# Kernel tuning notes

Measured on AMD Instinct MI355X. Metric: run time of the kernel, lower is better.

## Reference

```python
import jax, jax.numpy as jnp
import numpy as np
from jax import lax

WS = 11          # window_size
SIGMA = 1.5
CH = 3
PAD = WS // 2


def _depthwise_conv(x, w, groups):
    # x: [B, C, H, W], w: [C_out, C_in/groups, kh, kw]
    return lax.conv_general_dilated(
        x, w, window_strides=(1, 1), padding=[(PAD, PAD), (PAD, PAD)],
        feature_group_count=groups,
        dimension_numbers=("NCHW", "OIHW", "NCHW"))


def _make_window():
    xs = jnp.arange(WS, dtype=jnp.float32) - (WS // 2)
    g = jnp.exp(-(xs ** 2) / (2.0 * SIGMA ** 2))
    g = g / g.sum()
    w2d = jnp.outer(g, g)                       # [WS, WS]
    return jnp.broadcast_to(w2d, (CH, 1, WS, WS))  # depthwise kernel


def setup_inputs() -> dict:
    key = jax.random.key(0)
    k1, k2, k3 = jax.random.split(key, 3)
    B, H, W = 16, 512, 512
    img1 = jax.random.uniform(k1, (B, CH, H, W), dtype=jnp.float32)
    img2 = jax.random.uniform(k2, (B, CH, H, W), dtype=jnp.float32)
    match = jax.random.uniform(k3, (B, 1, H, W), dtype=jnp.float32)
    return {"img1": img1, "img2": img2, "match": match}


def reference(img1, img2, match):
    window = _make_window()
    box = jnp.ones((1, 1, WS, WS), dtype=jnp.float32) / (WS * WS)

    # mask from match map: box-filter then threshold
    m = _depthwise_conv(match, box, 1) + 1e-07
    mask = (m > 0.5).astype(jnp.float32) + 1e-07   # [B,1,H,W]

    mu1 = _depthwise_conv(img1, window, CH)
    mu2 = _depthwise_conv(img2, window, CH)
    mu1_sq = mu1 * mu1
    mu2_sq = mu2 * mu2
    mu1_mu2 = mu1 * mu2
    sigma1_sq = _depthwise_conv(img1 * img1, window, CH) - mu1_sq
    sigma2_sq = _depthwise_conv(img2 * img2, window, CH) - mu2_sq
    sigma12 = _depthwise_conv(img1 * img2, window, CH) - mu1_mu2

    C1 = 0.01 ** 2
    C2 = 0.03 ** 2
    ssim_map = ((2 * mu1_mu2 + C1) * (2 * sigma12 + C2)) / (
        (mu1_sq + mu2_sq + C1) * (sigma1_sq + sigma2_sq + C2))

    # mask [B,1,H,W] broadcasts over the 3 channels of ssim_map
    return jnp.sum((1.0 - ssim_map) * mask) / jnp.sum(mask) / 3.0
```

## Files before the change

kernel.cpp:

```cpp
#include <hip/hip_runtime.h>


#define BATCH 16
#define CHANS 3
#define IMH 512
#define IMW 512
#define STRIPW 64
#define STRIPH 256
#define RINGR 18
#define LDSW 84
#define SUP 8
#define NSUP (STRIPH / SUP)
#define NQ 20

__device__ __forceinline__ float4 ld4s(const float* p) { return *(const float4*)p; }
__device__ __forceinline__ void st4s(float* p, float4 v) { *(float4*)p = v; }
__device__ __forceinline__ void fma4(float4& a, float w, float4 x) {
    a.x = fmaf(w, x.x, a.x); a.y = fmaf(w, x.y, a.y);
    a.z = fmaf(w, x.z, a.z); a.w = fmaf(w, x.w, a.w);
}
__device__ __forceinline__ void fma4m(float4& a, float w, float4 x, float4 y) {
    a.x = fmaf(w, x.x * y.x, a.x); a.y = fmaf(w, x.y * y.y, a.y);
    a.z = fmaf(w, x.z * y.z, a.z); a.w = fmaf(w, x.w * y.w, a.w);
}
__device__ __forceinline__ void add4(float4& a, float4 x) {
    a.x += x.x; a.y += x.y; a.z += x.z; a.w += x.w;
}

__device__ __forceinline__ void convg(const float* __restrict__ row, int cb,
                                      const float* __restrict__ g, float out[4]) {
    float w[20];
    #pragma unroll
    for (int i = 0; i < 5; ++i) {
        float4 v = ld4s(row + cb + 4 * i);
        w[4*i+0] = v.x; w[4*i+1] = v.y; w[4*i+2] = v.z; w[4*i+3] = v.w;
    }
    #pragma unroll
    for (int j = 0; j < 4; ++j) {
        float a = 0.0f;
        #pragma unroll
        for (int k = 0; k < 11; ++k) a = fmaf(g[k], w[3 + j + k], a);
        out[j] = a;
    }
}

__device__ __forceinline__ void convb(const float* __restrict__ row, int cb,
                                      float out[4]) {
    float w[20];
    #pragma unroll
    for (int i = 0; i < 5; ++i) {
        float4 v = ld4s(row + cb + 4 * i);
        w[4*i+0] = v.x; w[4*i+1] = v.y; w[4*i+2] = v.z; w[4*i+3] = v.w;
    }
    #pragma unroll
    for (int j = 0; j < 4; ++j) {
        float a = 0.0f;
        #pragma unroll
        for (int k = 0; k < 11; ++k) a += w[3 + j + k];
        out[j] = a;
    }
}

__global__ __launch_bounds__(256) void ssim_main(
    const float* __restrict__ img1, const float* __restrict__ img2,
    const float* __restrict__ match, double* __restrict__ acc)
{
    __shared__ __align__(16) float ring1[RINGR][LDSW];
    __shared__ __align__(16) float ring2[RINGR][LDSW];
    __shared__ __align__(16) float ringm[RINGR][LDSW];
    __shared__ __align__(16) float fld[6][SUP][LDSW];
    __shared__ float redn[4], redd[4];

    const int tid = threadIdx.x;
    const int bc = blockIdx.z;
    const int b = bc / CHANS;
    const int c = bc - b * CHANS;
    const int ystart = blockIdx.y * STRIPH;
    const int bx0 = blockIdx.x * STRIPW - 8;

    const float* p1 = img1 + (size_t)(b * CHANS + c) * (IMH * IMW);
    const float* p2 = img2 + (size_t)(b * CHANS + c) * (IMH * IMW);
    const float* pm = match + (size_t)b * (IMH * IMW);

    float g[11];
    {
        float s = 0.0f;
        #pragma unroll
        for (int i = 0; i < 11; ++i) {
            float d = (float)(i - 5);
            g[i] = expf(-(d * d) / 4.5f);
            s += g[i];
        }
        #pragma unroll
        for (int i = 0; i < 11; ++i) g[i] /= s;
    }

    float num = 0.0f, den = 0.0f;

    auto stage = [&](int gy0, int nrows) {
        for (int t = tid; t < nrows * NQ; t += 256) {
            int r = t / NQ, q = t - r * NQ;
            int gy = gy0 + r;
            int slot = (gy + 36) % RINGR;
            int gx = bx0 + 4 * q;
            float4 v1, v2, vm;
            if ((unsigned)gy < IMH && (unsigned)gx <= (IMW - 4)) {
                const float* base = p1 + gy * IMW + gx;
                v1 = ld4s(base);
                v2 = ld4s(p2 + gy * IMW + gx);
                vm = ld4s(pm + gy * IMW + gx);
            } else if ((unsigned)gy < IMH) {
                float t1[4], t2[4], tm[4];
                #pragma unroll
                for (int e = 0; e < 4; ++e) {
                    int x = gx + e;
                    bool ok = (unsigned)x < IMW;
                    int off = gy * IMW + (ok ? x : 0);
                    t1[e] = ok ? p1[off] : 0.0f;
                    t2[e] = ok ? p2[off] : 0.0f;
                    tm[e] = ok ? pm[off] : 0.0f;
                }
                v1 = make_float4(t1[0], t1[1], t1[2], t1[3]);
                v2 = make_float4(t2[0], t2[1], t2[2], t2[3]);
                vm = make_float4(tm[0], tm[1], tm[2], tm[3]);
            } else {
                v1 = v2 = vm = make_float4(0.f, 0.f, 0.f, 0.f);
            }
            st4s(&ring1[slot][4 * q], v1);
            st4s(&ring2[slot][4 * q], v2);
            st4s(&ringm[slot][4 * q], vm);
        }
    };

    stage(ystart - 5, 10);

    for (int s = 0; s < NSUP; ++s) {
        const int ybase = ystart + s * SUP;

        stage(ybase + 5, SUP);
        __syncthreads();

        if (tid < SUP * NQ) {
            int r = tid / NQ, q = tid - r * NQ;
            int cq = 4 * q;
            int y = ybase + r;
            int sr = (y - 5 + 36) % RINGR;
            float4 a1 = make_float4(0,0,0,0), a2 = a1, a3 = a1,
                   a4 = a1, a5 = a1, am = a1;
            #pragma unroll
            for (int k = 0; k < 11; ++k) {
                float4 x1 = ld4s(&ring1[sr][cq]);
                float4 x2 = ld4s(&ring2[sr][cq]);
                float4 xm = ld4s(&ringm[sr][cq]);
                float w = g[k];
                fma4(a1, w, x1);
                fma4(a2, w, x2);
                fma4m(a3, w, x1, x1);
                fma4m(a4, w, x2, x2);
                fma4m(a5, w, x1, x2);
                add4(am, xm);
                sr++; if (sr >= RINGR) sr -= RINGR;
            }
            st4s(&fld[0][r][cq], a1);
            st4s(&fld[1][r][cq], a2);
            st4s(&fld[2][r][cq], a3);
            st4s(&fld[3][r][cq], a4);
            st4s(&fld[4][r][cq], a5);
            st4s(&fld[5][r][cq], am);
        }
        __syncthreads();

        if (tid < SUP * 16) {
            int r = tid >> 4, q = tid & 15;
            int cb = 4 * q;
            float mu1[4], mu2[4], m11[4], m22[4], m12[4], mb[4];
            convg(fld[0][r], cb, g, mu1);
            convg(fld[1][r], cb, g, mu2);
            convg(fld[2][r], cb, g, m11);
            convg(fld[3][r], cb, g, m22);
            convg(fld[4][r], cb, g, m12);
            convb(fld[5][r], cb, mb);
            #pragma unroll
            for (int j = 0; j < 4; ++j) {
                float mu1s = mu1[j] * mu1[j];
                float mu2s = mu2[j] * mu2[j];
                float mu12 = mu1[j] * mu2[j];
                float sg1  = m11[j] - mu1s;
                float sg2  = m22[j] - mu2s;
                float sg12 = m12[j] - mu12;
                float ssim = ((2.0f * mu12 + 1e-4f) * (2.0f * sg12 + 9e-4f)) /
                             ((mu1s + mu2s + 1e-4f) * (sg1 + sg2 + 9e-4f));
                float m = mb[j] * (1.0f / 121.0f) + 1e-7f;
                float mask = (m > 0.5f) ? (1.0f + 1e-7f) : 1e-7f;
                num += (1.0f - ssim) * mask;
                den += mask;
            }
        }
    }

    for (int off = 32; off > 0; off >>= 1) {
        num += __shfl_down(num, off);
        den += __shfl_down(den, off);
    }
    int wave = tid >> 6;
    int lane = tid & 63;
    if (lane == 0) { redn[wave] = num; redd[wave] = den; }
    __syncthreads();
    if (tid == 0) {
        float n = redn[0] + redn[1] + redn[2] + redn[3];
        atomicAdd(&acc[0], (double)n);
        if (c == 0) {
            float d = redd[0] + redd[1] + redd[2] + redd[3];
            atomicAdd(&acc[1], (double)d);
        }
    }
}

__global__ void init_acc(double* acc) {
    acc[0] = 0.0;
    acc[1] = 0.0;
}

__global__ void finalize(const double* __restrict__ acc, float* __restrict__ out) {
    out[0] = (float)(acc[0] / acc[1] / 3.0);
}

extern "C" void kernel_launch(void* const* d_in, const int* in_sizes, int n_in,
                              void* d_out, int out_size, void* d_ws, size_t ws_size,
                              hipStream_t stream) {
    const float* img1  = (const float*)d_in[0];
    const float* img2  = (const float*)d_in[1];
    const float* match = (const float*)d_in[2];
    float* out = (float*)d_out;
    double* acc = (double*)d_ws;

    init_acc<<<1, 1, 0, stream>>>(acc);

    dim3 grid(IMW / STRIPW, IMH / STRIPH, BATCH * CHANS);
    dim3 block(256, 1, 1);
    ssim_main<<<grid, block, 0, stream>>>(img1, img2, match, acc);

    finalize<<<1, 1, 0, stream>>>(acc, out);
}
```

Before: 245.5 us.

## Double super-row height, compute two rows per thread, widen horizontal pass, use partial-sum reduction

```diff
diff --git a/kernel.cpp b/kernel.cpp
--- a/kernel.cpp
+++ b/kernel.cpp
@@ -1,85 +1,52 @@
 #include <hip/hip_runtime.h>
 
 
-#define BATCH 16
-#define CHANS 3
 #define IMH 512
 #define IMW 512
-#define STRIPW 64
-#define STRIPH 256
-#define RINGR 18
-#define LDSW 84
-#define SUP 8
-#define NSUP (STRIPH / SUP)
-#define NQ 20
-
-__device__ __forceinline__ float4 ld4s(const float* p) { return *(const float4*)p; }
-__device__ __forceinline__ void st4s(float* p, float4 v) { *(float4*)p = v; }
+#define NCH 3
+#define SW 64
+#define SH 256
+#define SUPR 16
+#define NSUP (SH / SUPR)
+#define DATQ 20
+#define PITCH 84
+#define RS 26
+#define NBLK 768
+
+__device__ __forceinline__ float4 ld4(const float* p) { return *(const float4*)p; }
+__device__ __forceinline__ void st4(float* p, float4 v) { *(float4*)p = v; }
+__device__ __forceinline__ float4 mul4(float4 a, float4 b) {
+    return make_float4(a.x*b.x, a.y*b.y, a.z*b.z, a.w*b.w);
+}
 __device__ __forceinline__ void fma4(float4& a, float w, float4 x) {
     a.x = fmaf(w, x.x, a.x); a.y = fmaf(w, x.y, a.y);
     a.z = fmaf(w, x.z, a.z); a.w = fmaf(w, x.w, a.w);
 }
-__device__ __forceinline__ void fma4m(float4& a, float w, float4 x, float4 y) {
-    a.x = fmaf(w, x.x * y.x, a.x); a.y = fmaf(w, x.y * y.y, a.y);
-    a.z = fmaf(w, x.z * y.z, a.z); a.w = fmaf(w, x.w * y.w, a.w);
-}
 __device__ __forceinline__ void add4(float4& a, float4 x) {
     a.x += x.x; a.y += x.y; a.z += x.z; a.w += x.w;
 }
 
-__device__ __forceinline__ void convg(const float* __restrict__ row, int cb,
-                                      const float* __restrict__ g, float out[4]) {
-    float w[20];
-    #pragma unroll
-    for (int i = 0; i < 5; ++i) {
-        float4 v = ld4s(row + cb + 4 * i);
-        w[4*i+0] = v.x; w[4*i+1] = v.y; w[4*i+2] = v.z; w[4*i+3] = v.w;
-    }
-    #pragma unroll
-    for (int j = 0; j < 4; ++j) {
-        float a = 0.0f;
-        #pragma unroll
-        for (int k = 0; k < 11; ++k) a = fmaf(g[k], w[3 + j + k], a);
-        out[j] = a;
-    }
-}
-
-__device__ __forceinline__ void convb(const float* __restrict__ row, int cb,
-                                      float out[4]) {
-    float w[20];
-    #pragma unroll
-    for (int i = 0; i < 5; ++i) {
-        float4 v = ld4s(row + cb + 4 * i);
-        w[4*i+0] = v.x; w[4*i+1] = v.y; w[4*i+2] = v.z; w[4*i+3] = v.w;
-    }
-    #pragma unroll
-    for (int j = 0; j < 4; ++j) {
-        float a = 0.0f;
-        #pragma unroll
-        for (int k = 0; k < 11; ++k) a += w[3 + j + k];
-        out[j] = a;
-    }
-}
-
-__global__ __launch_bounds__(256) void ssim_main(
+__global__ __launch_bounds__(256, 2) void ssim_main(
     const float* __restrict__ img1, const float* __restrict__ img2,
-    const float* __restrict__ match, double* __restrict__ acc)
+    const float* __restrict__ match,
+    float* __restrict__ wsn, float* __restrict__ wsd,
+    double* __restrict__ acc, int use_partials)
 {
-    __shared__ __align__(16) float ring1[RINGR][LDSW];
-    __shared__ __align__(16) float ring2[RINGR][LDSW];
-    __shared__ __align__(16) float ringm[RINGR][LDSW];
-    __shared__ __align__(16) float fld[6][SUP][LDSW];
+    __shared__ __align__(16) float ring1[RS][PITCH];
+    __shared__ __align__(16) float ring2[RS][PITCH];
+    __shared__ __align__(16) float ringm[RS][PITCH];
+    __shared__ __align__(16) float fld[6][SUPR][PITCH];
     __shared__ float redn[4], redd[4];
 
     const int tid = threadIdx.x;
     const int bc = blockIdx.z;
-    const int b = bc / CHANS;
-    const int c = bc - b * CHANS;
-    const int ystart = blockIdx.y * STRIPH;
-    const int bx0 = blockIdx.x * STRIPW - 8;
-
-    const float* p1 = img1 + (size_t)(b * CHANS + c) * (IMH * IMW);
-    const float* p2 = img2 + (size_t)(b * CHANS + c) * (IMH * IMW);
+    const int b = bc / NCH;
+    const int c = bc - b * NCH;
+    const int ystart = blockIdx.y * SH;
+    const int bx0 = blockIdx.x * SW - 8;
+
+    const float* p1 = img1 + (size_t)(b * NCH + c) * (IMH * IMW);
+    const float* p2 = img2 + (size_t)(b * NCH + c) * (IMH * IMW);
     const float* pm = match + (size_t)b * (IMH * IMW);
 
     float g[11];
@@ -98,17 +65,17 @@
     float num = 0.0f, den = 0.0f;
 
     auto stage = [&](int gy0, int nrows) {
-        for (int t = tid; t < nrows * NQ; t += 256) {
-            int r = t / NQ, q = t - r * NQ;
+        for (int t = tid; t < nrows * DATQ; t += 256) {
+            int r = t / DATQ, q = t - r * DATQ;
             int gy = gy0 + r;
-            int slot = (gy + 36) % RINGR;
+            int slot = (gy + 520) % RS;
             int gx = bx0 + 4 * q;
             float4 v1, v2, vm;
-            if ((unsigned)gy < IMH && (unsigned)gx <= (IMW - 4)) {
-                const float* base = p1 + gy * IMW + gx;
-                v1 = ld4s(base);
-                v2 = ld4s(p2 + gy * IMW + gx);
-                vm = ld4s(pm + gy * IMW + gx);
+            if ((unsigned)gy < IMH && gx >= 0 && gx <= (IMW - 4)) {
+                int off = gy * IMW + gx;
+                v1 = ld4(p1 + off);
+                v2 = ld4(p2 + off);
+                vm = ld4(pm + off);
             } else if ((unsigned)gy < IMH) {
                 float t1[4], t2[4], tm[4];
                 #pragma unroll
@@ -126,73 +93,115 @@
             } else {
                 v1 = v2 = vm = make_float4(0.f, 0.f, 0.f, 0.f);
             }
-            st4s(&ring1[slot][4 * q], v1);
-            st4s(&ring2[slot][4 * q], v2);
-            st4s(&ringm[slot][4 * q], vm);
+            st4(&ring1[slot][4 * q], v1);
+            st4(&ring2[slot][4 * q], v2);
+            st4(&ringm[slot][4 * q], vm);
         }
     };
 
     stage(ystart - 5, 10);
 
     for (int s = 0; s < NSUP; ++s) {
-        const int ybase = ystart + s * SUP;
-
-        stage(ybase + 5, SUP);
+        const int ybase = ystart + s * SUPR;
+
+        stage(ybase + 5, SUPR);
         __syncthreads();
 
-        if (tid < SUP * NQ) {
-            int r = tid / NQ, q = tid - r * NQ;
+        if (tid < 160) {
+            int q = tid % DATQ, pr = tid / DATQ;
             int cq = 4 * q;
-            int y = ybase + r;
-            int sr = (y - 5 + 36) % RINGR;
-            float4 a1 = make_float4(0,0,0,0), a2 = a1, a3 = a1,
-                   a4 = a1, a5 = a1, am = a1;
-            #pragma unroll
-            for (int k = 0; k < 11; ++k) {
-                float4 x1 = ld4s(&ring1[sr][cq]);
-                float4 x2 = ld4s(&ring2[sr][cq]);
-                float4 xm = ld4s(&ringm[sr][cq]);
-                float w = g[k];
-                fma4(a1, w, x1);
-                fma4(a2, w, x2);
-                fma4m(a3, w, x1, x1);
-                fma4m(a4, w, x2, x2);
-                fma4m(a5, w, x1, x2);
-                add4(am, xm);
-                sr++; if (sr >= RINGR) sr -= RINGR;
-            }
-            st4s(&fld[0][r][cq], a1);
-            st4s(&fld[1][r][cq], a2);
-            st4s(&fld[2][r][cq], a3);
-            st4s(&fld[3][r][cq], a4);
-            st4s(&fld[4][r][cq], a5);
-            st4s(&fld[5][r][cq], am);
+            int y0 = ybase + 2 * pr;
+            int sv = (y0 - 5 + 520) % RS;
+            float4 A0[6], A1[6];
+            #pragma unroll
+            for (int f = 0; f < 6; ++f) {
+                A0[f] = make_float4(0.f, 0.f, 0.f, 0.f);
+                A1[f] = make_float4(0.f, 0.f, 0.f, 0.f);
+            }
+            #pragma unroll
+            for (int k = 0; k < 12; ++k) {
+                int sr = sv + k; if (sr >= RS) sr -= RS;
+                float4 x1 = ld4(&ring1[sr][cq]);
+                float4 x2 = ld4(&ring2[sr][cq]);
+                float4 xm = ld4(&ringm[sr][cq]);
+                float4 p11 = mul4(x1, x1);
+                float4 p22 = mul4(x2, x2);
+                float4 p12 = mul4(x1, x2);
+                if (k < 11) {
+                    float w = g[k];
+                    fma4(A0[0], w, x1);  fma4(A0[1], w, x2);
+                    fma4(A0[2], w, p11); fma4(A0[3], w, p22);
+                    fma4(A0[4], w, p12); add4(A0[5], xm);
+                }
+                if (k > 0) {
+                    float w = g[k - 1];
+                    fma4(A1[0], w, x1);  fma4(A1[1], w, x2);
+                    fma4(A1[2], w, p11); fma4(A1[3], w, p22);
+                    fma4(A1[4], w, p12); add4(A1[5], xm);
+                }
+            }
+            int r0 = 2 * pr;
+            #pragma unroll
+            for (int f = 0; f < 6; ++f) {
+                st4(&fld[f][r0][cq], A0[f]);
+                st4(&fld[f][r0 + 1][cq], A1[f]);
+            }
         }
         __syncthreads();
 
-        if (tid < SUP * 16) {
-            int r = tid >> 4, q = tid & 15;
-            int cb = 4 * q;
-            float mu1[4], mu2[4], m11[4], m22[4], m12[4], mb[4];
-            convg(fld[0][r], cb, g, mu1);
-            convg(fld[1][r], cb, g, mu2);
-            convg(fld[2][r], cb, g, m11);
-            convg(fld[3][r], cb, g, m22);
-            convg(fld[4][r], cb, g, m12);
-            convb(fld[5][r], cb, mb);
-            #pragma unroll
-            for (int j = 0; j < 4; ++j) {
-                float mu1s = mu1[j] * mu1[j];
-                float mu2s = mu2[j] * mu2[j];
-                float mu12 = mu1[j] * mu2[j];
-                float sg1  = m11[j] - mu1s;
-                float sg2  = m22[j] - mu2s;
-                float sg12 = m12[j] - mu12;
-                float ssim = ((2.0f * mu12 + 1e-4f) * (2.0f * sg12 + 9e-4f)) /
-                             ((mu1s + mu2s + 1e-4f) * (sg1 + sg2 + 9e-4f));
-                float m = mb[j] * (1.0f / 121.0f) + 1e-7f;
+        if (tid < 64) {
+            int r = tid >> 2, gc = tid & 3;
+            int base = 16 * gc;
+            float W[32];
+            auto loadW = [&](int f) {
+                #pragma unroll
+                for (int i = 0; i < 8; ++i) {
+                    float4 v = ld4(&fld[f][r][base + 4 * i]);
+                    W[4*i] = v.x; W[4*i+1] = v.y; W[4*i+2] = v.z; W[4*i+3] = v.w;
+                }
+            };
+            auto convW = [&](float* out) {
+                #pragma unroll
+                for (int j = 0; j < 16; ++j) {
+                    float a = 0.0f;
+                    #pragma unroll
+                    for (int k = 0; k < 11; ++k) a = fmaf(g[k], W[j + 3 + k], a);
+                    out[j] = a;
+                }
+            };
+            float mu1[16]; loadW(0); convW(mu1);
+            float mu2[16]; loadW(1); convW(mu2);
+            float S1[16];  loadW(2); convW(S1);
+            #pragma unroll
+            for (int j = 0; j < 16; ++j) S1[j] -= mu1[j] * mu1[j];
+            float D2[16];  loadW(3); convW(D2);
+            #pragma unroll
+            for (int j = 0; j < 16; ++j)
+                D2[j] = (D2[j] - mu2[j] * mu2[j]) + S1[j] + 9e-4f;
+            float N2[16];  loadW(4); convW(N2);
+            #pragma unroll
+            for (int j = 0; j < 16; ++j)
+                N2[j] = 2.0f * (N2[j] - mu1[j] * mu2[j]) + 9e-4f;
+            float N1[16], D1[16];
+            #pragma unroll
+            for (int j = 0; j < 16; ++j) {
+                N1[j] = 2.0f * mu1[j] * mu2[j] + 1e-4f;
+                D1[j] = mu1[j] * mu1[j] + mu2[j] * mu2[j] + 1e-4f;
+            }
+            float MB[16];  loadW(5);
+            #pragma unroll
+            for (int j = 0; j < 16; ++j) {
+                float a = 0.0f;
+                #pragma unroll
+                for (int k = 0; k < 11; ++k) a += W[j + 3 + k];
+                MB[j] = a;
+            }
+            #pragma unroll
+            for (int j = 0; j < 16; ++j) {
+                float ssim = (N1[j] * N2[j]) / (D1[j] * D2[j]);
+                float m = fmaf(MB[j], (1.0f / 121.0f), 1e-7f);
                 float mask = (m > 0.5f) ? (1.0f + 1e-7f) : 1e-7f;
-                num += (1.0f - ssim) * mask;
+                num = fmaf(1.0f - ssim, mask, num);
                 den += mask;
             }
         }
@@ -208,20 +217,47 @@
     __syncthreads();
     if (tid == 0) {
         float n = redn[0] + redn[1] + redn[2] + redn[3];
-        atomicAdd(&acc[0], (double)n);
-        if (c == 0) {
-            float d = redd[0] + redd[1] + redd[2] + redd[3];
-            atomicAdd(&acc[1], (double)d);
-        }
-    }
-}
-
-__global__ void init_acc(double* acc) {
-    acc[0] = 0.0;
-    acc[1] = 0.0;
-}
-
-__global__ void finalize(const double* __restrict__ acc, float* __restrict__ out) {
+        float d = redd[0] + redd[1] + redd[2] + redd[3];
+        if (use_partials) {
+            int bid = (blockIdx.z * gridDim.y + blockIdx.y) * gridDim.x + blockIdx.x;
+            wsn[bid] = n;
+            wsd[bid] = d;
+        } else {
+            atomicAdd(&acc[0], (double)n);
+            if (c == 0) atomicAdd(&acc[1], (double)d);
+        }
+    }
+}
+
+__global__ void finalize_partials(const float* __restrict__ wsn,
+                                  const float* __restrict__ wsd,
+                                  float* __restrict__ out) {
+    __shared__ double rn[4], rd[4];
+    int tid = threadIdx.x;
+    double num = 0.0, den = 0.0;
+    for (int i = tid; i < NBLK; i += 256) {
+        num += (double)wsn[i];
+        int z = i >> 4;
+        if (z % NCH == 0) den += (double)wsd[i];
+    }
+    for (int off = 32; off > 0; off >>= 1) {
+        num += __shfl_down(num, off);
+        den += __shfl_down(den, off);
+    }
+    int wave = tid >> 6, lane = tid & 63;
+    if (lane == 0) { rn[wave] = num; rd[wave] = den; }
+    __syncthreads();
+    if (tid == 0) {
+        num = rn[0] + rn[1] + rn[2] + rn[3];
+        den = rd[0] + rd[1] + rd[2] + rd[3];
+        out[0] = (float)(num / den / 3.0);
+    }
+}
+
+__global__ void init_acc(double* acc) { acc[0] = 0.0; acc[1] = 0.0; }
+
+__global__ void finalize_atomic(const double* __restrict__ acc,
+                                float* __restrict__ out) {
     out[0] = (float)(acc[0] / acc[1] / 3.0);
 }
 
@@ -232,13 +268,23 @@
     const float* img2  = (const float*)d_in[1];
     const float* match = (const float*)d_in[2];
     float* out = (float*)d_out;
-    double* acc = (double*)d_ws;
-
-    init_acc<<<1, 1, 0, stream>>>(acc);
-
-    dim3 grid(IMW / STRIPW, IMH / STRIPH, BATCH * CHANS);
+
+    dim3 grid(IMW / SW, IMH / SH, 16 * NCH);
     dim3 block(256, 1, 1);
-    ssim_main<<<grid, block, 0, stream>>>(img1, img2, match, acc);
-
-    finalize<<<1, 1, 0, stream>>>(acc, out);
-}
+
+    int use_partials = (ws_size >= (size_t)(2 * NBLK * sizeof(float))) ? 1 : 0;
+    if (use_partials) {
+        float* wsn = (float*)d_ws;
+        float* wsd = wsn + NBLK;
+        ssim_main<<<grid, block, 0, stream>>>(img1, img2, match, wsn, wsd,
+                                              (double*)nullptr, 1);
+        finalize_partials<<<1, 256, 0, stream>>>(wsn, wsd, out);
+    } else {
+        double* acc = (double*)d_ws;
+        init_acc<<<1, 1, 0, stream>>>(acc);
+        ssim_main<<<grid, block, 0, stream>>>(img1, img2, match,
+                                              (float*)nullptr, (float*)nullptr,
+                                              acc, 0);
+        finalize_atomic<<<1, 1, 0, stream>>>(acc, out);
+    }
+}
```

Result: slower. 311.8 us (+27.0%).
